# Performance work log

Hardware: AMD Instinct MI355X
Metric: run time of the kernel (lower is better)

Reference implementation:

```python
import jax, jax.numpy as jnp
import numpy as np

DN = ('NCHW', 'OIHW', 'NCHW')

def _conv(x, W, pad):
    return jax.lax.conv_general_dilated(x, W, (1, 1), [(pad, pad), (pad, pad)], dimension_numbers=DN)

def _cbs(x, W, s, b, pad):
    # Conv2d(bias=False) + folded BatchNorm (scale/bias) + SiLU
    y = _conv(x, W, pad) * s[None, :, None, None] + b[None, :, None, None]
    return y * jax.nn.sigmoid(y)

def _l2norm(x):
    n = jnp.sqrt(jnp.sum(x * x, axis=1, keepdims=True))
    return x / jnp.maximum(n, 1e-12)

def setup_inputs() -> dict:
    key = jax.random.key(0)
    ks = jax.random.split(key, 24)
    B, C, H, L, TD, NC = 16, 256, 64, 40, 768, 8
    EMB = (TD + NC * 2) // 2  # 392
    w = lambda k, sh: jax.random.normal(k, sh, jnp.float32) * 0.02
    img = jax.random.normal(ks[0], (B, C, H, H), jnp.float32)
    flang = jax.random.normal(ks[1], (B, L, TD), jnp.float32)
    lengths = jax.random.randint(ks[2], (B, 1), 5, L + 1)
    word_mask = (jnp.arange(L)[None, :] < lengths).astype(jnp.int32)
    return {
        'img': img, 'flang': flang, 'word_mask': word_mask, 'sigma_w': 0.1,
        'W1': w(ks[3], (EMB, TD)), 'b1': w(ks[4], (EMB,)),
        'W2': w(ks[5], (NC * 2, EMB)), 'b2': w(ks[6], (NC * 2,)),
        'Wv': w(ks[7], (C, C, 1, 1)), 'sv': jnp.ones((C,)), 'bv': w(ks[8], (C,)),
        'Wg': w(ks[9], (NC, NC, 1, 1)), 'sg': jnp.ones((NC,)), 'bg': w(ks[10], (NC,)),
        'Wb': w(ks[11], (NC, NC, 1, 1)), 'sb': jnp.ones((NC,)), 'bb': w(ks[12], (NC,)),
        'Wf1': w(ks[13], (C, C, 1, 1)), 'sf1': jnp.ones((C,)), 'bf1': w(ks[14], (C,)),
        'Wf2': w(ks[15], (C, C, 3, 3)), 'sf2': jnp.ones((C,)), 'bf2': w(ks[16], (C,)),
        'Wf3': w(ks[17], (C, C, 1, 1)), 'bf3': w(ks[18], (C,)),
        'Ws': w(ks[19], (NC, C, 3, 3)), 'bs': w(ks[20], (NC,)),
        'add_weight': jnp.zeros((), jnp.float32),
    }

def reference(img, flang, word_mask, sigma_w, W1, b1, W2, b2, Wv, sv, bv,
              Wg, sg, bg, Wb, sb, bb, Wf1, sf1, bf1, Wf2, sf2, bf2,
              Wf3, bf3, Ws, bs, add_weight):
    B, C, H = img.shape[0], img.shape[1], img.shape[2]
    nc = Wg.shape[0]
    map_visu = jnp.tanh(_cbs(img, Wv, sv, bv, 0))
    # ragged masked mean excluding first (CLS) and last (SEP) masked tokens
    m = word_mask.astype(jnp.float32)
    c = jnp.cumsum(m, axis=1)
    tot = c[:, -1:]
    inc = m * ((c > 1) & (c < tot)).astype(jnp.float32)  # [B,L]
    flang_avg = jnp.sum(flang * inc[:, :, None], axis=1) / jnp.sum(inc, axis=1, keepdims=True)
    map_flang = jax.nn.sigmoid((flang_avg @ W1.T + b1) @ W2.T + b2)  # [B,2*nc]
    maps = map_flang.reshape(B, nc, 2)
    sigma_x = sigma_w * H
    sig = _conv(img, Ws, 0) + bs[None, :, None, None]  # [B,nc,H-2,H-2]
    sigma_weight = jax.nn.sigmoid(jnp.mean(sig, axis=(2, 3), keepdims=True))  # [B,nc,1,1]
    sigma_y = sigma_x * sigma_weight
    yc = (maps[:, :, 0] * H).astype(jnp.int32).astype(jnp.float32)[:, :, None, None]
    xc = (maps[:, :, 1] * H).astype(jnp.int32).astype(jnp.float32)[:, :, None, None]
    gy = jnp.arange(H, dtype=jnp.float32)[None, None, :, None]
    gx = jnp.arange(H, dtype=jnp.float32)[None, None, None, :]
    weights = jnp.exp(-((gy - yc) ** 2 / (2.0 * sigma_y ** 2) + (gx - xc) ** 2 / (2.0 * sigma_x ** 2)))  # [B,nc,H,H]
    gamma = jnp.tanh(_cbs(weights, Wg, sg, bg, 0))
    beta = jnp.tanh(_cbs(weights, Wb, sb, bb, 0))
    g = jnp.mean(gamma, axis=1, keepdims=True)
    bmax = jnp.max(beta, axis=1, keepdims=True)
    v_film = _l2norm(g * map_visu + bmax)
    v_film = _cbs(v_film, Wf1, sf1, bf1, 0)
    v_film = _cbs(v_film, Wf2, sf2, bf2, 1)
    v_film = _conv(v_film, Wf3, 0) + bf3[None, :, None, None]
    aw = jnp.tanh(add_weight)
    v_add = (1.0 + aw) * img + (1.0 - aw) * v_film
    return _l2norm(v_add)
```

## Files before the change

kernel.cpp:

```cpp
#include <hip/hip_runtime.h>
#include <hip/hip_bf16.h>


#define DEVFN static __device__ __forceinline__

DEVFN float sigmoidf_(float x) { return 1.f / (1.f + expf(-x)); }
DEVFN float siluf_(float y) { return y / (1.f + __expf(-y)); }
DEVFN float tanh_fast_(float x) { return 1.f - 2.f / (__expf(2.f * x) + 1.f); }

typedef __attribute__((ext_vector_type(8))) short bf16x8;
typedef __attribute__((ext_vector_type(4))) float f32x4;

DEVFN unsigned short f2bf_(float f) {
    union { __hip_bfloat16 b; unsigned short u; } cv;
    cv.b = __float2bfloat16(f);
    return cv.u;
}
DEVFN float bf2f_(unsigned short u) {
    union { unsigned short u; __hip_bfloat16 b; } cv;
    cv.u = u;
    return __bfloat162float(cv.b);
}

__global__ void prep_kernel(const float* __restrict__ Wv, const float* __restrict__ Wf1,
                            const float* __restrict__ Wf3, const float* __restrict__ Wf2,
                            short* __restrict__ WvB, short* __restrict__ W1B,
                            short* __restrict__ W3B, short* __restrict__ WB2) {
    int idx = blockIdx.x * 256 + threadIdx.x;
    if (idx < 65536) {
        int j    = idx & 7;
        int lane = (idx >> 3) & 63;
        int coT  = (idx >> 9) & 15;
        int ci32 = (idx >> 13) & 7;
        int co = coT * 16 + (lane & 15);
        int ci = ci32 * 32 + ((lane >> 4) << 3) + j;
        int src = co * 256 + ci;
        WvB[idx] = (short)f2bf_(Wv[src]);
        W1B[idx] = (short)f2bf_(Wf1[src]);
        W3B[idx] = (short)f2bf_(Wf3[src]);
    }
    int o = idx - 65536;
    if (o >= 0 && o < 589824) {
        int j    = o & 7;
        int lane = (o >> 3) & 63;
        int coT  = (o >> 9) & 15;
        int ci32 = (o >> 13) & 7;
        int kk   = o >> 16;
        int co = coT * 16 + (lane & 15);
        int ci = ci32 * 32 + ((lane >> 4) << 3) + j;
        WB2[o] = (short)f2bf_(Wf2[(co * 256 + ci) * 9 + kk]);
    }
}

__global__ void lang_kernel(const float* __restrict__ flang, const int* __restrict__ mask,
                            float* __restrict__ fa) {
    __shared__ float inc[40];
    __shared__ float isum;
    int b = blockIdx.x, t = threadIdx.x;
    if (t == 0) {
        float cum[40];
        float c = 0.f;
        for (int l = 0; l < 40; ++l) { c += (float)mask[b * 40 + l]; cum[l] = c; }
        float tot = c, s = 0.f;
        for (int l = 0; l < 40; ++l) {
            float m = (float)mask[b * 40 + l];
            float v = (cum[l] > 1.f && cum[l] < tot) ? m : 0.f;
            inc[l] = v; s += v;
        }
        isum = s;
    }
    __syncthreads();
    for (int d = t; d < 768; d += 256) {
        float a = 0.f;
        for (int l = 0; l < 40; ++l) a += flang[(size_t)(b * 40 + l) * 768 + d] * inc[l];
        fa[b * 768 + d] = a / isum;
    }
}

__global__ void mlp_kernel(const float* __restrict__ fa_g, const float* __restrict__ W1,
                           const float* __restrict__ b1, const float* __restrict__ W2,
                           const float* __restrict__ b2, float* __restrict__ ycxc) {
    __shared__ float fa[768];
    __shared__ float h[392];
    __shared__ float o[16];
    int b = blockIdx.x, t = threadIdx.x;
    for (int k = t; k < 768; k += 448) fa[k] = fa_g[b * 768 + k];
    __syncthreads();
    if (t < 392) {
        float a = b1[t];
        const float* w = W1 + (size_t)t * 768;
        for (int k = 0; k < 768; ++k) a = fmaf(fa[k], w[k], a);
        h[t] = a;
    }
    __syncthreads();
    if (t < 16) {
        float a = b2[t];
        const float* w = W2 + (size_t)t * 392;
        for (int k = 0; k < 392; ++k) a = fmaf(h[k], w[k], a);
        o[t] = sigmoidf_(a);
    }
    __syncthreads();
    if (t < 8) {
        ycxc[b * 8 + t]       = (float)(int)(o[2 * t] * 64.f);
        ycxc[128 + b * 8 + t] = (float)(int)(o[2 * t + 1] * 64.f);
    }
}

__global__ void wsum_kernel(const float* __restrict__ img, float* __restrict__ S) {
    __shared__ float red[9 * 256];
    int bc = blockIdx.x;
    int t = threadIdx.x;
    float s[9];
#pragma unroll
    for (int k = 0; k < 9; ++k) s[k] = 0.f;
    const float* p = img + (size_t)bc * 4096;
    for (int j = 0; j < 16; ++j) {
        int idx = t + j * 256;
        int y = idx >> 6, x = idx & 63;
        float v = p[idx];
#pragma unroll
        for (int ky = 0; ky < 3; ++ky) {
            if (y < ky || y > ky + 61) continue;
#pragma unroll
            for (int kx = 0; kx < 3; ++kx) {
                if (x < kx || x > kx + 61) continue;
                s[ky * 3 + kx] += v;
            }
        }
    }
#pragma unroll
    for (int k = 0; k < 9; ++k) red[k * 256 + t] = s[k];
    __syncthreads();
    for (int st = 128; st > 0; st >>= 1) {
        if (t < st) {
#pragma unroll
            for (int k = 0; k < 9; ++k) red[k * 256 + t] += red[k * 256 + t + st];
        }
        __syncthreads();
    }
    if (t < 9) S[(size_t)bc * 9 + t] = red[t * 256];
}

__global__ void sigw_kernel(const float* __restrict__ Ws, const float* __restrict__ S,
                            const float* __restrict__ bs, float* __restrict__ sigw) {
    __shared__ float red[8 * 256];
    int b = blockIdx.x, t = threadIdx.x;
    float sv[9];
    const float* Sp = S + (size_t)(b * 256 + t) * 9;
#pragma unroll
    for (int k = 0; k < 9; ++k) sv[k] = Sp[k];
#pragma unroll
    for (int co = 0; co < 8; ++co) {
        const float* wp = Ws + (size_t)(co * 256 + t) * 9;
        float a = 0.f;
#pragma unroll
        for (int k = 0; k < 9; ++k) a = fmaf(wp[k], sv[k], a);
        red[co * 256 + t] = a;
    }
    __syncthreads();
    for (int st = 128; st > 0; st >>= 1) {
        if (t < st) {
#pragma unroll
            for (int co = 0; co < 8; ++co) red[co * 256 + t] += red[co * 256 + t + st];
        }
        __syncthreads();
    }
    if (t < 8) sigw[b * 8 + t] = sigmoidf_(red[t * 256] / 3844.f + bs[t]);
}

__global__ void gauss_kernel(const float* __restrict__ ycxc, const float* __restrict__ sigw,
                             const float* __restrict__ sigma_w,
                             const float* __restrict__ Wg, const float* __restrict__ sg,
                             const float* __restrict__ bg,
                             const float* __restrict__ Wb, const float* __restrict__ sb,
                             const float* __restrict__ bb,
                             float* __restrict__ g, float* __restrict__ bm) {
    int blk = blockIdx.x;
    int b = blk >> 6, y = blk & 63;
    int x = threadIdx.x;
    float sx = sigma_w[0] * 64.f;
    float w[8];
#pragma unroll
    for (int n = 0; n < 8; ++n) {
        float yc = ycxc[b * 8 + n], xc = ycxc[128 + b * 8 + n];
        float sy = sx * sigw[b * 8 + n];
        float dy = (float)y - yc, dx = (float)x - xc;
        w[n] = expf(-(dy * dy / (2.f * sy * sy) + dx * dx / (2.f * sx * sx)));
    }
    float gacc = 0.f, bmax = -3.4e38f;
#pragma unroll
    for (int n = 0; n < 8; ++n) {
        float a1 = 0.f, a2 = 0.f;
#pragma unroll
        for (int m = 0; m < 8; ++m) {
            a1 = fmaf(Wg[n * 8 + m], w[m], a1);
            a2 = fmaf(Wb[n * 8 + m], w[m], a2);
        }
        float ga = tanhf(siluf_(a1 * sg[n] + bg[n]));
        float be = tanhf(siluf_(a2 * sb[n] + bb[n]));
        gacc += ga;
        bmax = fmaxf(bmax, be);
    }
    g[(size_t)(b * 64 + y) * 64 + x] = gacc * 0.125f;
    bm[(size_t)(b * 64 + y) * 64 + x] = bmax;
}

__global__ __launch_bounds__(256) void f01_kernel(
        const float* __restrict__ img, const short* __restrict__ wvb,
        const short* __restrict__ w1b,
        const float* __restrict__ sv, const float* __restrict__ bv,
        const float* __restrict__ s1, const float* __restrict__ b1,
        const float* __restrict__ g, const float* __restrict__ bm,
        __hip_bfloat16* __restrict__ outB) {
    __shared__ __attribute__((aligned(16))) short lA[64 * 264];
    __shared__ float invs[64];
    __shared__ float ls_sv[256], ls_bv[256], ls_s1[256], ls_b1[256];
    __shared__ float ls_g[64], ls_bm[64];
    float* pr = (float*)lA;
    int blk = blockIdx.x, b = blk >> 6, y = blk & 63;
    int t = threadIdx.x, w = t >> 6, lane = t & 63;
    int lx = lane & 15, koct = lane >> 4;

    ls_sv[t] = sv[t]; ls_bv[t] = bv[t];
    ls_s1[t] = s1[t]; ls_b1[t] = b1[t];
    if (t < 64) {
        ls_g[t]  = g[(size_t)(b * 64 + y) * 64 + t];
        ls_bm[t] = bm[(size_t)(b * 64 + y) * 64 + t];
    }

    {
        int x = t & 63, cg = t >> 6;
        const float* ib = img + (size_t)b * 1048576 + y * 64 + x;
#pragma unroll
        for (int c8 = 0; c8 < 8; ++c8) {
            int ci0 = cg * 64 + c8 * 8;
            unsigned short r[8];
#pragma unroll
            for (int j = 0; j < 8; ++j) r[j] = f2bf_(ib[(size_t)(ci0 + j) * 4096]);
            *(uint4*)&lA[x * 264 + ci0] = *(uint4*)r;
        }
    }
    f32x4 acc[4][4];
#pragma unroll
    for (int mi = 0; mi < 4; ++mi)
#pragma unroll
        for (int ni = 0; ni < 4; ++ni) acc[mi][ni] = (f32x4){0.f, 0.f, 0.f, 0.f};
    __syncthreads();

#pragma unroll
    for (int k32 = 0; k32 < 8; ++k32) {
        const short* wp = wvb + (((k32 * 16) + w * 4) * 64 + lane) * 8;
        bf16x8 bfr[4];
#pragma unroll
        for (int ni = 0; ni < 4; ++ni) bfr[ni] = *(const bf16x8*)(wp + ni * 512);
        bf16x8 afr[4];
#pragma unroll
        for (int mi = 0; mi < 4; ++mi)
            afr[mi] = *(const bf16x8*)&lA[(mi * 16 + lx) * 264 + k32 * 32 + koct * 8];
#pragma unroll
        for (int mi = 0; mi < 4; ++mi)
#pragma unroll
            for (int ni = 0; ni < 4; ++ni)
                acc[mi][ni] = __builtin_amdgcn_mfma_f32_16x16x32_bf16(afr[mi], bfr[ni], acc[mi][ni], 0, 0, 0);
    }
    __syncthreads();

#pragma unroll
    for (int mi = 0; mi < 4; ++mi)
#pragma unroll
        for (int rr = 0; rr < 4; ++rr) {
            int x = mi * 16 + koct * 4 + rr;
            float ps = 0.f;
#pragma unroll
            for (int ni = 0; ni < 4; ++ni) {
                int co = w * 64 + ni * 16 + lx;
                float yv = fmaf(acc[mi][ni][rr], ls_sv[co], ls_bv[co]);
                float mvv = tanh_fast_(siluf_(yv));
                float v = fmaf(ls_g[x], mvv, ls_bm[x]);
                acc[mi][ni][rr] = v;
                ps += v * v;
            }
            pr[x * 64 + w * 16 + lx] = ps;
        }
    __syncthreads();
    if (t < 64) {
        float s2 = 0.f;
        for (int q = 0; q < 64; ++q) s2 += pr[t * 64 + q];
        invs[t] = 1.f / fmaxf(sqrtf(s2), 1e-12f);
    }
    __syncthreads();

#pragma unroll
    for (int mi = 0; mi < 4; ++mi)
#pragma unroll
        for (int ni = 0; ni < 4; ++ni) {
            int co = w * 64 + ni * 16 + lx;
#pragma unroll
            for (int rr = 0; rr < 4; ++rr) {
                int x = mi * 16 + koct * 4 + rr;
                lA[x * 264 + co] = (short)f2bf_(acc[mi][ni][rr] * invs[x]);
            }
        }
#pragma unroll
    for (int mi = 0; mi < 4; ++mi)
#pragma unroll
        for (int ni = 0; ni < 4; ++ni) acc[mi][ni] = (f32x4){0.f, 0.f, 0.f, 0.f};
    __syncthreads();

#pragma unroll
    for (int k32 = 0; k32 < 8; ++k32) {
        const short* wp = w1b + (((k32 * 16) + w * 4) * 64 + lane) * 8;
        bf16x8 bfr[4];
#pragma unroll
        for (int ni = 0; ni < 4; ++ni) bfr[ni] = *(const bf16x8*)(wp + ni * 512);
        bf16x8 afr[4];
#pragma unroll
        for (int mi = 0; mi < 4; ++mi)
            afr[mi] = *(const bf16x8*)&lA[(mi * 16 + lx) * 264 + k32 * 32 + koct * 8];
#pragma unroll
        for (int mi = 0; mi < 4; ++mi)
#pragma unroll
            for (int ni = 0; ni < 4; ++ni)
                acc[mi][ni] = __builtin_amdgcn_mfma_f32_16x16x32_bf16(afr[mi], bfr[ni], acc[mi][ni], 0, 0, 0);
    }
    __syncthreads();

#pragma unroll
    for (int mi = 0; mi < 4; ++mi)
#pragma unroll
        for (int ni = 0; ni < 4; ++ni) {
            int co = w * 64 + ni * 16 + lx;
#pragma unroll
            for (int rr = 0; rr < 4; ++rr) {
                int x = mi * 16 + koct * 4 + rr;
                float yv = fmaf(acc[mi][ni][rr], ls_s1[co], ls_b1[co]);
                lA[x * 264 + co] = (short)f2bf_(siluf_(yv));
            }
        }
    __syncthreads();
    unsigned short* og = (unsigned short*)outB + (size_t)(b * 64 + y) * 16384;
#pragma unroll
    for (int it = 0; it < 8; ++it) {
        int e8 = t + it * 256;
        int x2 = e8 >> 5, c8 = e8 & 31;
        *(uint4*)(og + e8 * 8) = *(uint4*)&lA[x2 * 264 + c8 * 8];
    }
}

__global__ __launch_bounds__(256, 2) void conv3x3_mfma(const __hip_bfloat16* __restrict__ xin,
                                                       const short* __restrict__ wb,
                                                       const float* __restrict__ sc,
                                                       const float* __restrict__ bi,
                                                       __hip_bfloat16* __restrict__ outB) {
    __shared__ __attribute__((aligned(16))) short lds[4 * 66 * 72];
    int blk = blockIdx.x;
    int b = blk >> 5, y0 = (blk & 31) * 2;
    int t = threadIdx.x;
    int w = t >> 6, lane = t & 63;
    int lx = lane & 15, koct = lane >> 4;
    const unsigned short* xg = (const unsigned short*)xin + (size_t)b * 1048576;

    int goff[9], loff[9];
    bool uval[9], uin[9];
#pragma unroll
    for (int p = 0; p < 9; ++p) {
        int u = t + p * 256;
        uval[p] = (u < 2112);
        int r = u / 528;
        int rem = u - r * 528;
        int xp = rem >> 3, ci8 = rem & 7;
        int ys = y0 + r - 1, xs = xp - 1;
        uin[p] = uval[p] && ys >= 0 && ys < 64 && xs >= 0 && xs < 64;
        goff[p] = (ys * 64 + xs) * 256 + ci8 * 8;
        loff[p] = (r * 66 + xp) * 72 + ci8 * 8;
    }
    uint4 pf[9];

    f32x4 acc[8][4];
#pragma unroll
    for (int mi = 0; mi < 8; ++mi)
#pragma unroll
        for (int ni = 0; ni < 4; ++ni) acc[mi][ni] = (f32x4){0.f, 0.f, 0.f, 0.f};

#pragma unroll
    for (int p = 0; p < 9; ++p) {
        uint4 v = {0u, 0u, 0u, 0u};
        if (uin[p]) v = *(const uint4*)(xg + goff[p]);
        pf[p] = v;
    }
#pragma unroll
    for (int p = 0; p < 9; ++p)
        if (uval[p]) *(uint4*)&lds[loff[p]] = pf[p];
    __syncthreads();

    for (int cc = 0; cc < 4; ++cc) {
        if (cc < 3) {
#pragma unroll
            for (int p = 0; p < 9; ++p) {
                uint4 v = {0u, 0u, 0u, 0u};
                if (uin[p]) v = *(const uint4*)(xg + goff[p] + (cc + 1) * 64);
                pf[p] = v;
            }
        }
#pragma unroll
        for (int kk = 0; kk < 9; ++kk) {
            int ky = kk / 3, kx = kk - ky * 3;
#pragma unroll
            for (int k32 = 0; k32 < 2; ++k32) {
                const short* wp = wb + ((((kk * 8 + cc * 2 + k32) * 16) + w * 4) * 64 + lane) * 8;
                bf16x8 bfr[4];
#pragma unroll
                for (int ni = 0; ni < 4; ++ni)
                    bfr[ni] = *(const bf16x8*)(wp + ni * 512);
                bf16x8 afr[8];
#pragma unroll
                for (int mi = 0; mi < 8; ++mi) {
                    int row = mi >> 2, xb = (mi & 3) * 16;
                    afr[mi] = *(const bf16x8*)&lds[((row + ky) * 66 + xb + lx + kx) * 72 + k32 * 32 + koct * 8];
                }
#pragma unroll
                for (int mi = 0; mi < 8; ++mi)
#pragma unroll
                    for (int ni = 0; ni < 4; ++ni)
                        acc[mi][ni] = __builtin_amdgcn_mfma_f32_16x16x32_bf16(afr[mi], bfr[ni], acc[mi][ni], 0, 0, 0);
            }
        }
        __syncthreads();
        if (cc < 3) {
#pragma unroll
            for (int p = 0; p < 9; ++p)
                if (uval[p]) *(uint4*)&lds[loff[p]] = pf[p];
            __syncthreads();
        }
    }
#pragma unroll
    for (int r2 = 0; r2 < 2; ++r2) {
#pragma unroll
        for (int mi4 = 0; mi4 < 4; ++mi4) {
            int mi = r2 * 4 + mi4;
#pragma unroll
            for (int ni = 0; ni < 4; ++ni) {
                int co = w * 64 + ni * 16 + lx;
                float s = sc[co], bb2 = bi[co];
#pragma unroll
                for (int rr = 0; rr < 4; ++rr) {
                    int x = mi4 * 16 + koct * 4 + rr;
                    float yv = fmaf(acc[mi][ni][rr], s, bb2);
                    lds[x * 264 + co] = (short)f2bf_(siluf_(yv));
                }
            }
        }
        __syncthreads();
        unsigned short* og = (unsigned short*)outB + (size_t)(b * 64 + y0 + r2) * 16384;
#pragma unroll
        for (int it = 0; it < 8; ++it) {
            int e8 = t + it * 256;
            int x2 = e8 >> 5, c8 = e8 & 31;
            *(uint4*)(og + e8 * 8) = *(uint4*)&lds[x2 * 264 + c8 * 8];
        }
        __syncthreads();
    }
}

__global__ __launch_bounds__(256, 4) void final_mfma(const __hip_bfloat16* __restrict__ inB,
                                                     const short* __restrict__ w3b,
                                                     const float* __restrict__ bf3,
                                                     const float* __restrict__ img,
                                                     const float* __restrict__ addw,
                                                     float* __restrict__ outF) {
    __shared__ __attribute__((aligned(16))) short lA[64 * 264];
    __shared__ float pr2[256];
    __shared__ float invs[64];
    __shared__ float ls_b[256];
    int blk = blockIdx.x, b = blk >> 6, y = blk & 63;
    int t = threadIdx.x, w = t >> 6, lane = t & 63;
    int lx = lane & 15, koct = lane >> 4;
    ls_b[t] = bf3[t];

    const unsigned short* xg = (const unsigned short*)inB + (size_t)(b * 64 + y) * 16384;
#pragma unroll
    for (int it = 0; it < 8; ++it) {
        int e8 = t + it * 256;
        int x2 = e8 >> 5, c8 = e8 & 31;
        *(uint4*)&lA[x2 * 264 + c8 * 8] = *(const uint4*)(xg + e8 * 8);
    }
    f32x4 acc[4][4];
#pragma unroll
    for (int mi = 0; mi < 4; ++mi)
#pragma unroll
        for (int ni = 0; ni < 4; ++ni) acc[mi][ni] = (f32x4){0.f, 0.f, 0.f, 0.f};
    __syncthreads();

#pragma unroll
    for (int k32 = 0; k32 < 8; ++k32) {
        const short* wp = w3b + (((k32 * 16) + w * 4) * 64 + lane) * 8;
        bf16x8 bfr[4];
#pragma unroll
        for (int ni = 0; ni < 4; ++ni) bfr[ni] = *(const bf16x8*)(wp + ni * 512);
        bf16x8 afr[4];
#pragma unroll
        for (int mi = 0; mi < 4; ++mi)
            afr[mi] = *(const bf16x8*)&lA[(mi * 16 + lx) * 264 + k32 * 32 + koct * 8];
#pragma unroll
        for (int mi = 0; mi < 4; ++mi)
#pragma unroll
            for (int ni = 0; ni < 4; ++ni)
                acc[mi][ni] = __builtin_amdgcn_mfma_f32_16x16x32_bf16(afr[mi], bfr[ni], acc[mi][ni], 0, 0, 0);
    }
    __syncthreads();

#pragma unroll
    for (int mi = 0; mi < 4; ++mi)
#pragma unroll
        for (int ni = 0; ni < 4; ++ni) {
            int co = w * 64 + ni * 16 + lx;
            float b3 = ls_b[co];
#pragma unroll
            for (int rr = 0; rr < 4; ++rr) {
                int x = mi * 16 + koct * 4 + rr;
                lA[co * 66 + x] = (short)f2bf_(acc[mi][ni][rr] + b3);
            }
        }
    __syncthreads();

    float aw = tanhf(addw[0]);
    float ca = 1.f + aw, cb = 1.f - aw;
    int x = t & 63, cg = t >> 6;
    const float* ip = img + (size_t)b * 1048576 + y * 64 + x;
    float ss = 0.f;
#pragma unroll 8
    for (int j = 0; j < 64; ++j) {
        int co = cg * 64 + j;
        float v = fmaf(cb, bf2f_((unsigned short)lA[co * 66 + x]), ca * ip[(size_t)co * 4096]);
        ss += v * v;
    }
    pr2[cg * 64 + x] = ss;
    __syncthreads();
    if (t < 64)
        invs[t] = 1.f / fmaxf(sqrtf(pr2[t] + pr2[64 + t] + pr2[128 + t] + pr2[192 + t]), 1e-12f);
    __syncthreads();
    float iv = invs[x];
    float* op = outF + (size_t)b * 1048576 + y * 64 + x;
#pragma unroll 8
    for (int j = 0; j < 64; ++j) {
        int co = cg * 64 + j;
        float v = fmaf(cb, bf2f_((unsigned short)lA[co * 66 + x]), ca * ip[(size_t)co * 4096]);
        op[(size_t)co * 4096] = v * iv;
    }
}

extern "C" void kernel_launch(void* const* d_in, const int* in_sizes, int n_in,
                              void* d_out, int out_size, void* d_ws, size_t ws_size,
                              hipStream_t stream) {
    const float* img     = (const float*)d_in[0];
    const float* flang   = (const float*)d_in[1];
    const int*   wmask   = (const int*)d_in[2];
    const float* sigma_w = (const float*)d_in[3];
    const float* W1      = (const float*)d_in[4];
    const float* b1      = (const float*)d_in[5];
    const float* W2      = (const float*)d_in[6];
    const float* b2      = (const float*)d_in[7];
    const float* Wv      = (const float*)d_in[8];
    const float* sv      = (const float*)d_in[9];
    const float* bv      = (const float*)d_in[10];
    const float* Wg      = (const float*)d_in[11];
    const float* sg      = (const float*)d_in[12];
    const float* bg      = (const float*)d_in[13];
    const float* Wb      = (const float*)d_in[14];
    const float* sb      = (const float*)d_in[15];
    const float* bb      = (const float*)d_in[16];
    const float* Wf1     = (const float*)d_in[17];
    const float* sf1     = (const float*)d_in[18];
    const float* bf1     = (const float*)d_in[19];
    const float* Wf2     = (const float*)d_in[20];
    const float* sf2     = (const float*)d_in[21];
    const float* bf2     = (const float*)d_in[22];
    const float* Wf3     = (const float*)d_in[23];
    const float* bf3     = (const float*)d_in[24];
    const float* Ws      = (const float*)d_in[25];
    const float* bs      = (const float*)d_in[26];
    const float* addw    = (const float*)d_in[27];
    float* out = (float*)d_out;
    float* ws  = (float*)d_ws;

    short* WvB  = (short*)ws;
    short* W1B  = (short*)(ws + 32768);
    short* W3B  = (short*)(ws + 65536);
    short* WB2  = (short*)(ws + 98304);
    float* fa   = ws + 393216;
    float* ycxc = ws + 405504;
    float* S    = ws + 405760;
    float* sigw = ws + 442624;
    float* gmap = ws + 442752;
    float* bmap = ws + 508288;
    __hip_bfloat16* bufA = (__hip_bfloat16*)(ws + 573824);
    __hip_bfloat16* bufB = (__hip_bfloat16*)(ws + 8962432);

    prep_kernel<<<2560, 256, 0, stream>>>(Wv, Wf1, Wf3, Wf2, WvB, W1B, W3B, WB2);
    lang_kernel<<<16, 256, 0, stream>>>(flang, wmask, fa);
    mlp_kernel<<<16, 448, 0, stream>>>(fa, W1, b1, W2, b2, ycxc);
    wsum_kernel<<<4096, 256, 0, stream>>>(img, S);
    sigw_kernel<<<16, 256, 0, stream>>>(Ws, S, bs, sigw);
    gauss_kernel<<<1024, 64, 0, stream>>>(ycxc, sigw, sigma_w, Wg, sg, bg, Wb, sb, bb, gmap, bmap);
    f01_kernel<<<1024, 256, 0, stream>>>(img, WvB, W1B, sv, bv, sf1, bf1, gmap, bmap, bufB);
    conv3x3_mfma<<<512, 256, 0, stream>>>(bufB, WB2, sf2, bf2, bufA);
    final_mfma<<<1024, 256, 0, stream>>>(bufA, W3B, bf3, img, addw, out);
}
```

Measured before the change: 467.9 us.

## Double-buffer conv3x3 LDS staging with async global-to-LDS loads; fuse lang and MLP

The 3x3 conv kernel now keeps two LDS buffers and fills the next channel chunk with direct global-to-LDS copies (global_load_lds) while the current chunk is being computed. This replaces the old register prefetch and the extra barrier-separated LDS store. Out-of-bounds halo and padding slots load from a small zeroed workspace buffer, which prep_kernel clears. The language-pooling and MLP kernels are merged into one launch, which drops a launch and a global round-trip for the pooled features. In exchange the conv kernel doubles its LDS footprint, which could limit occupancy. It also relies on the async copies having completed at each barrier.

```diff
diff --git a/kernel.cpp b/kernel.cpp
--- a/kernel.cpp
+++ b/kernel.cpp
@@ -22,11 +22,19 @@
     return __bfloat162float(cv.b);
 }
 
+DEVFN void async_cp16(const void* g, void* l) {
+    __builtin_amdgcn_global_load_lds(
+        (const __attribute__((address_space(1))) unsigned int*)g,
+        (__attribute__((address_space(3))) unsigned int*)l, 16, 0, 0);
+}
+
 __global__ void prep_kernel(const float* __restrict__ Wv, const float* __restrict__ Wf1,
                             const float* __restrict__ Wf3, const float* __restrict__ Wf2,
                             short* __restrict__ WvB, short* __restrict__ W1B,
-                            short* __restrict__ W3B, short* __restrict__ WB2) {
+                            short* __restrict__ W3B, short* __restrict__ WB2,
+                            float* __restrict__ zbuf) {
     int idx = blockIdx.x * 256 + threadIdx.x;
+    if (idx < 8) zbuf[idx] = 0.f;
     if (idx < 65536) {
         int j    = idx & 7;
         int lane = (idx >> 3) & 63;
@@ -52,10 +60,15 @@
     }
 }
 
-__global__ void lang_kernel(const float* __restrict__ flang, const int* __restrict__ mask,
-                            float* __restrict__ fa) {
+__global__ void langmlp_kernel(const float* __restrict__ flang, const int* __restrict__ mask,
+                               const float* __restrict__ W1, const float* __restrict__ b1,
+                               const float* __restrict__ W2, const float* __restrict__ b2,
+                               float* __restrict__ ycxc) {
     __shared__ float inc[40];
     __shared__ float isum;
+    __shared__ float fa[768];
+    __shared__ float h[392];
+    __shared__ float o[16];
     int b = blockIdx.x, t = threadIdx.x;
     if (t == 0) {
         float cum[40];
@@ -70,21 +83,11 @@
         isum = s;
     }
     __syncthreads();
-    for (int d = t; d < 768; d += 256) {
+    for (int d = t; d < 768; d += 448) {
         float a = 0.f;
         for (int l = 0; l < 40; ++l) a += flang[(size_t)(b * 40 + l) * 768 + d] * inc[l];
-        fa[b * 768 + d] = a / isum;
-    }
-}
-
-__global__ void mlp_kernel(const float* __restrict__ fa_g, const float* __restrict__ W1,
-                           const float* __restrict__ b1, const float* __restrict__ W2,
-                           const float* __restrict__ b2, float* __restrict__ ycxc) {
-    __shared__ float fa[768];
-    __shared__ float h[392];
-    __shared__ float o[16];
-    int b = blockIdx.x, t = threadIdx.x;
-    for (int k = t; k < 768; k += 448) fa[k] = fa_g[b * 768 + k];
+        fa[d] = a / isum;
+    }
     __syncthreads();
     if (t < 392) {
         float a = b1[t];
@@ -347,34 +350,39 @@
     }
 }
 
+DEVFN void stage_chunk(const unsigned short* __restrict__ xg, short* ldsbuf,
+                       const unsigned short* __restrict__ zbuf, int cc, int y0, int t) {
+#pragma unroll
+    for (int p = 0; p < 10; ++p) {
+        int slot = t + p * 256;
+        if (slot < 2376) {
+            int r = slot / 594;
+            int rem = slot - r * 594;
+            int xp = rem / 9;
+            int oct = rem - xp * 9;
+            int ys = y0 + r - 1, xs = xp - 1;
+            bool valid = (oct < 8) && (ys >= 0) && (ys < 64) && (xs >= 0) && (xs < 64);
+            const unsigned short* gp = valid ? (xg + ((ys * 64 + xs) * 256 + cc * 64 + oct * 8))
+                                             : zbuf;
+            async_cp16(gp, ldsbuf + slot * 8);
+        }
+    }
+}
+
 __global__ __launch_bounds__(256, 2) void conv3x3_mfma(const __hip_bfloat16* __restrict__ xin,
                                                        const short* __restrict__ wb,
                                                        const float* __restrict__ sc,
                                                        const float* __restrict__ bi,
+                                                       const float* __restrict__ zbufF,
                                                        __hip_bfloat16* __restrict__ outB) {
-    __shared__ __attribute__((aligned(16))) short lds[4 * 66 * 72];
+    __shared__ __attribute__((aligned(16))) short lds[2][19008];
     int blk = blockIdx.x;
     int b = blk >> 5, y0 = (blk & 31) * 2;
     int t = threadIdx.x;
     int w = t >> 6, lane = t & 63;
     int lx = lane & 15, koct = lane >> 4;
     const unsigned short* xg = (const unsigned short*)xin + (size_t)b * 1048576;
-
-    int goff[9], loff[9];
-    bool uval[9], uin[9];
-#pragma unroll
-    for (int p = 0; p < 9; ++p) {
-        int u = t + p * 256;
-        uval[p] = (u < 2112);
-        int r = u / 528;
-        int rem = u - r * 528;
-        int xp = rem >> 3, ci8 = rem & 7;
-        int ys = y0 + r - 1, xs = xp - 1;
-        uin[p] = uval[p] && ys >= 0 && ys < 64 && xs >= 0 && xs < 64;
-        goff[p] = (ys * 64 + xs) * 256 + ci8 * 8;
-        loff[p] = (r * 66 + xp) * 72 + ci8 * 8;
-    }
-    uint4 pf[9];
+    const unsigned short* zbuf = (const unsigned short*)zbufF;
 
     f32x4 acc[8][4];
 #pragma unroll
@@ -382,27 +390,12 @@
 #pragma unroll
         for (int ni = 0; ni < 4; ++ni) acc[mi][ni] = (f32x4){0.f, 0.f, 0.f, 0.f};
 
-#pragma unroll
-    for (int p = 0; p < 9; ++p) {
-        uint4 v = {0u, 0u, 0u, 0u};
-        if (uin[p]) v = *(const uint4*)(xg + goff[p]);
-        pf[p] = v;
-    }
-#pragma unroll
-    for (int p = 0; p < 9; ++p)
-        if (uval[p]) *(uint4*)&lds[loff[p]] = pf[p];
+    stage_chunk(xg, lds[0], zbuf, 0, y0, t);
     __syncthreads();
 
     for (int cc = 0; cc < 4; ++cc) {
-        if (cc < 3) {
-#pragma unroll
-            for (int p = 0; p < 9; ++p) {
-                uint4 v = {0u, 0u, 0u, 0u};
-                if (uin[p]) v = *(const uint4*)(xg + goff[p] + (cc + 1) * 64);
-                pf[p] = v;
-            }
-        }
-#pragma unroll
+        short* cur = lds[cc & 1];
+        if (cc < 3) stage_chunk(xg, lds[(cc + 1) & 1], zbuf, cc + 1, y0, t);
         for (int kk = 0; kk < 9; ++kk) {
             int ky = kk / 3, kx = kk - ky * 3;
 #pragma unroll
@@ -416,7 +409,7 @@
 #pragma unroll
                 for (int mi = 0; mi < 8; ++mi) {
                     int row = mi >> 2, xb = (mi & 3) * 16;
-                    afr[mi] = *(const bf16x8*)&lds[((row + ky) * 66 + xb + lx + kx) * 72 + k32 * 32 + koct * 8];
+                    afr[mi] = *(const bf16x8*)&cur[((row + ky) * 66 + xb + lx + kx) * 72 + k32 * 32 + koct * 8];
                 }
 #pragma unroll
                 for (int mi = 0; mi < 8; ++mi)
@@ -426,13 +419,8 @@
             }
         }
         __syncthreads();
-        if (cc < 3) {
-#pragma unroll
-            for (int p = 0; p < 9; ++p)
-                if (uval[p]) *(uint4*)&lds[loff[p]] = pf[p];
-            __syncthreads();
-        }
-    }
+    }
+    short* ep = &lds[0][0];
 #pragma unroll
     for (int r2 = 0; r2 < 2; ++r2) {
 #pragma unroll
@@ -446,7 +434,7 @@
                 for (int rr = 0; rr < 4; ++rr) {
                     int x = mi4 * 16 + koct * 4 + rr;
                     float yv = fmaf(acc[mi][ni][rr], s, bb2);
-                    lds[x * 264 + co] = (short)f2bf_(siluf_(yv));
+                    ep[x * 264 + co] = (short)f2bf_(siluf_(yv));
                 }
             }
         }
@@ -456,7 +444,7 @@
         for (int it = 0; it < 8; ++it) {
             int e8 = t + it * 256;
             int x2 = e8 >> 5, c8 = e8 & 31;
-            *(uint4*)(og + e8 * 8) = *(uint4*)&lds[x2 * 264 + c8 * 8];
+            *(uint4*)(og + e8 * 8) = *(uint4*)&ep[x2 * 264 + c8 * 8];
         }
         __syncthreads();
     }
@@ -587,22 +575,21 @@
     short* W1B  = (short*)(ws + 32768);
     short* W3B  = (short*)(ws + 65536);
     short* WB2  = (short*)(ws + 98304);
-    float* fa   = ws + 393216;
     float* ycxc = ws + 405504;
     float* S    = ws + 405760;
     float* sigw = ws + 442624;
     float* gmap = ws + 442752;
     float* bmap = ws + 508288;
-    __hip_bfloat16* bufA = (__hip_bfloat16*)(ws + 573824);
-    __hip_bfloat16* bufB = (__hip_bfloat16*)(ws + 8962432);
-
-    prep_kernel<<<2560, 256, 0, stream>>>(Wv, Wf1, Wf3, Wf2, WvB, W1B, W3B, WB2);
-    lang_kernel<<<16, 256, 0, stream>>>(flang, wmask, fa);
-    mlp_kernel<<<16, 448, 0, stream>>>(fa, W1, b1, W2, b2, ycxc);
+    float* zbuf = ws + 573824;
+    __hip_bfloat16* bufA = (__hip_bfloat16*)(ws + 573840);
+    __hip_bfloat16* bufB = (__hip_bfloat16*)(ws + 8962448);
+
+    prep_kernel<<<2560, 256, 0, stream>>>(Wv, Wf1, Wf3, Wf2, WvB, W1B, W3B, WB2, zbuf);
+    langmlp_kernel<<<16, 448, 0, stream>>>(flang, wmask, W1, b1, W2, b2, ycxc);
     wsum_kernel<<<4096, 256, 0, stream>>>(img, S);
     sigw_kernel<<<16, 256, 0, stream>>>(Ws, S, bs, sigw);
     gauss_kernel<<<1024, 64, 0, stream>>>(ycxc, sigw, sigma_w, Wg, sg, bg, Wb, sb, bb, gmap, bmap);
     f01_kernel<<<1024, 256, 0, stream>>>(img, WvB, W1B, sv, bv, sf1, bf1, gmap, bmap, bufB);
-    conv3x3_mfma<<<512, 256, 0, stream>>>(bufB, WB2, sf2, bf2, bufA);
+    conv3x3_mfma<<<512, 256, 0, stream>>>(bufB, WB2, sf2, bf2, zbuf, bufA);
     final_mfma<<<1024, 256, 0, stream>>>(bufA, W3B, bf3, img, addw, out);
 }
```

New measurement: 419.5 us. -10.3%, faster.
